# Kernel optimization log

Measured on AMD Instinct MI355X. Metric: run time of the kernel, lower is better.

## Reference

```python
import jax, jax.numpy as jnp
import numpy as np

B, T, D, TY = 64, 512, 96, 512
H, DK = 4, 32            # num_heads, embed_dim_per_head
E = H * DK               # embed_dim = 128
P = 2                    # function='L' -> 2 coefficients
L, HID = 64, 128         # latent_dim, hidden_dim


def setup_inputs() -> dict:
    key = jax.random.key(0)
    ks = jax.random.split(key, 16)
    inp = {
        "timesteps": jax.random.uniform(ks[0], (B, T), jnp.float32),
        "X": jax.random.normal(ks[1], (B, T, D), jnp.float32),
        "M": jax.random.randint(ks[2], (B, T, D), 0, 2).astype(jnp.float32),
        "y_time_steps": jax.random.uniform(ks[3], (B, TY), jnp.float32),
        # time_embedding: Linear(1, E)
        "te_w": jax.random.normal(ks[4], (E,), jnp.float32),
        "te_b": jax.random.normal(ks[5], (E,), jnp.float32) * 0.1,
        # learned query [1, P, E]
        "query": jax.random.normal(ks[6], (1, P, E), jnp.float32),
        # query_map / key_map: Linear(E, E), stored [in, out]
        "q_w": jax.random.normal(ks[7], (E, E), jnp.float32) / np.sqrt(E),
        "q_b": jax.random.normal(ks[8], (E,), jnp.float32) * 0.1,
        "k_w": jax.random.normal(ks[9], (E, E), jnp.float32) / np.sqrt(E),
        "k_b": jax.random.normal(ks[10], (E,), jnp.float32) * 0.1,
        # attn shared out: Linear(2D*H, L)
        "ow": jax.random.normal(ks[11], (2 * D * H, L), jnp.float32) / np.sqrt(2 * D * H),
        "ob": jnp.zeros((L,), jnp.float32),
        # decoder MLP: Linear(L,HID)+ReLU+Linear(HID,D)
        "w1": jax.random.normal(ks[12], (L, HID), jnp.float32) / np.sqrt(L),
        "b1": jnp.zeros((HID,), jnp.float32),
        "w2": jax.random.normal(ks[13], (HID, D), jnp.float32) / np.sqrt(HID),
        "b2": jnp.zeros((D,), jnp.float32),
    }
    return inp


def _fld_forward(timesteps, X, M, y_time_steps, te_w, te_b, query,
                 q_w, q_b, k_w, k_b, ow, ob, w1, b1, w2, b2):
    b, t, d = X.shape
    # time embedding: Linear(1,E), sin applied to indices i % H == 0
    emb = timesteps[..., None] * te_w + te_b               # [B,T,E]
    sin_idx = (jnp.arange(E) % H) == 0
    emb = jnp.where(sin_idx, jnp.sin(emb), emb)

    X_cat = jnp.concatenate([X, M], axis=-1)               # [B,T,2D]
    M_cat = jnp.concatenate([M, M], axis=-1)               # [B,T,2D]

    q = query @ q_w + q_b                                   # [1,P,E]
    k = emb @ k_w + k_b                                     # [B,T,E]
    q = q.reshape(1, P, H, DK).transpose(0, 2, 1, 3)        # [1,H,P,dk]
    k = k.reshape(b, t, H, DK).transpose(0, 2, 1, 3)        # [B,H,T,dk]

    scores = jnp.einsum('xhpd,bhtd->bhpt', q, k) / np.sqrt(DK)  # [B,H,P,T]
    # broadcast over value feature dim, mask per-feature, softmax over T
    logits = jnp.where(M_cat[:, None, None, :, :] == 0, -jnp.inf,
                       scores[..., None])                   # [B,H,P,T,2D]
    p = jax.nn.softmax(logits, axis=-2)
    xa = jnp.einsum('bhptf,btf->bhpf', p, X_cat)            # [B,H,P,2D]
    xa = xa.transpose(0, 2, 1, 3).reshape(b, P, H * 2 * d)  # [B,P,H*2D]
    coeffs = xa @ ow + ob                                   # [B,P,L]

    # function 'L': linear in y_time_steps
    x = coeffs[:, 0][:, None, :] + y_time_steps[:, :, None] * coeffs[:, 1][:, None, :]
    h1 = jax.nn.relu(x @ w1 + b1)
    return h1 @ w2 + b2                                     # [B,TY,D]


def reference(timesteps, X, M, y_time_steps, te_w, te_b, query,
              q_w, q_b, k_w, k_b, ow, ob, w1, b1, w2, b2):
    return _fld_forward(timesteps, X, M, y_time_steps, te_w, te_b, query,
                        q_w, q_b, k_w, k_b, ow, ob, w1, b1, w2, b2)
```

## Files before the change

kernel.cpp:

```cpp
#include <hip/hip_runtime.h>
#include <math.h>

#define B_   64
#define T_   512
#define D_   96
#define TY_  512
#define H_   4
#define DK_  32
#define E_   128
#define P_   2
#define L_   64
#define HID_ 128

#define WS_W2Q   0
#define WS_BQ    1024
#define WS_OB2   1056
#define WS_PN    2048
#define WS_PD    395264
#define WS_AB    788480

__global__ __launch_bounds__(256) void kprep(
    const float* __restrict__ query, const float* __restrict__ q_w,
    const float* __restrict__ q_b,   const float* __restrict__ k_w,
    const float* __restrict__ k_b,   const float* __restrict__ ow,
    const float* __restrict__ ob,    float* __restrict__ ws)
{
    const int tid = threadIdx.x;
    if (blockIdx.x == 0) {
        __shared__ float qm[P_ * E_];
        {
            int p = tid >> 7, ep = tid & 127;
            float acc = q_b[ep];
            #pragma unroll 4
            for (int e = 0; e < E_; ++e)
                acc += query[p * E_ + e] * q_w[e * E_ + ep];
            qm[p * E_ + ep] = acc;
        }
        __syncthreads();
        const float rs = 0.17677669529663687f;
        for (int idx = tid; idx < E_ * 8; idx += 256) {
            int e = idx >> 3, hp = idx & 7, h = hp >> 1, p = hp & 1;
            float acc = 0.f;
            #pragma unroll
            for (int dk = 0; dk < DK_; ++dk)
                acc += k_w[e * E_ + h * DK_ + dk] * qm[p * E_ + h * DK_ + dk];
            ws[WS_W2Q + idx] = acc * rs;
        }
        if (tid < 8) {
            int hp = tid, h = hp >> 1, p = hp & 1;
            float acc = 0.f;
            #pragma unroll
            for (int dk = 0; dk < DK_; ++dk)
                acc += k_b[h * DK_ + dk] * qm[p * E_ + h * DK_ + dk];
            ws[WS_BQ + hp] = acc * rs;
        }
    } else {
        __shared__ float obred[4][64];
        int l = tid & 63, sl = tid >> 6;
        float acc = 0.f;
        #pragma unroll 4
        for (int j = 0; j < D_; ++j)
            acc += ow[(size_t)(sl * 2 * D_ + D_ + j) * L_ + l];
        obred[sl][l] = acc;
        __syncthreads();
        if (sl == 0)
            ws[WS_OB2 + l] = ob[l] + obred[0][l] + obred[1][l] + obred[2][l] + obred[3][l];
    }
}

__global__ __launch_bounds__(256) void kspool(
    const float* __restrict__ tsteps, const float* __restrict__ te_w,
    const float* __restrict__ te_b,   const float* __restrict__ X,
    const float* __restrict__ M,      float* __restrict__ ws)
{
    const int c = blockIdx.x, b = blockIdx.y, tid = threadIdx.x;
    __shared__ float w2q_s[E_ * 8];
    __shared__ float tw_s[E_], tb_s[E_], bq_s[8];
    __shared__ float w_s[64 * 8];
    __shared__ float red[96 * 17];

    #pragma unroll
    for (int i = 0; i < 4; ++i) w2q_s[tid + i * 256] = ws[WS_W2Q + tid + i * 256];
    if (tid < E_) { tw_s[tid] = te_w[tid]; tb_s[tid] = te_b[tid]; }
    if (tid < 8)  bq_s[tid] = ws[WS_BQ + tid];
    __syncthreads();

    {
        const int t = tid & 63, hpg = tid >> 6, hp0 = hpg * 2;
        const float tv = tsteps[b * T_ + c * 64 + t];
        float a0 = 0.f, a1 = 0.f;
        #pragma unroll 4
        for (int e = 0; e < E_; ++e) {
            float v = tv * tw_s[e] + tb_s[e];
            if ((e & 3) == 0) v = __sinf(v);
            float2 w = *(const float2*)&w2q_s[e * 8 + hp0];
            a0 += v * w.x;
            a1 += v * w.y;
        }
        w_s[t * 8 + hp0]     = __expf(a0 + bq_s[hp0]);
        w_s[t * 8 + hp0 + 1] = __expf(a1 + bq_s[hp0 + 1]);
    }
    __syncthreads();

    const int fid = tid & 127, slice = tid >> 7;
    float num[8] = {0.f, 0.f, 0.f, 0.f, 0.f, 0.f, 0.f, 0.f};
    float den[8] = {0.f, 0.f, 0.f, 0.f, 0.f, 0.f, 0.f, 0.f};
    if (fid < 96) {
        #pragma unroll 4
        for (int i = 0; i < 32; ++i) {
            int tl = slice + 2 * i;
            size_t base = ((size_t)(b * T_ + c * 64 + tl)) * D_ + fid;
            float m = M[base], x = X[base];
            float mx = m * x;
            const float* wr = w_s + tl * 8;
            #pragma unroll
            for (int hp = 0; hp < 8; ++hp) {
                num[hp] += wr[hp] * mx;
                den[hp] += wr[hp] * m;
            }
        }
    }
    __syncthreads();
    if (slice == 1 && fid < 96) {
        #pragma unroll
        for (int hp = 0; hp < 8; ++hp) {
            red[fid * 17 + hp]     = num[hp];
            red[fid * 17 + 8 + hp] = den[hp];
        }
    }
    __syncthreads();
    if (slice == 0 && fid < 96) {
        float* pN = ws + WS_PN + ((size_t)((b * 8 + c) * 8)) * 96;
        float* pD = ws + WS_PD + ((size_t)((b * 8 + c) * 8)) * 96;
        #pragma unroll
        for (int hp = 0; hp < 8; ++hp) {
            pN[hp * 96 + fid] = num[hp] + red[fid * 17 + hp];
            pD[hp * 96 + fid] = den[hp] + red[fid * 17 + 8 + hp];
        }
    }
}

__global__ __launch_bounds__(256) void kcoef(
    const float* __restrict__ ow, const float* __restrict__ w1,
    const float* __restrict__ b1, float* __restrict__ ws)
{
    const int b = blockIdx.x, tid = threadIdx.x;
    __shared__ float xa_s[8 * 96];
    __shared__ float cf_part[2 * 128];
    __shared__ float cf_s[2 * 64];

    for (int flat = tid; flat < 8 * 96; flat += 256) {
        int hp = flat / 96, f = flat - hp * 96;
        float n = 0.f, d = 0.f;
        #pragma unroll
        for (int c = 0; c < 8; ++c) {
            n += ws[WS_PN + ((size_t)((b * 8 + c) * 8 + hp)) * 96 + f];
            d += ws[WS_PD + ((size_t)((b * 8 + c) * 8 + hp)) * 96 + f];
        }
        xa_s[flat] = n / d;
    }
    __syncthreads();
    {
        int hh = tid >> 7, rem = tid & 127, p = rem >> 6, l = rem & 63;
        float acc = (hh == 0) ? ws[WS_OB2 + l] : 0.f;
        #pragma unroll
        for (int hi = 0; hi < 2; ++hi) {
            int h = hh * 2 + hi;
            const float* xr = xa_s + (h * 2 + p) * 96;
            const float* owr = ow + (size_t)(h * 2 * D_) * L_ + l;
            #pragma unroll 4
            for (int f = 0; f < 96; ++f)
                acc += xr[f] * owr[(size_t)f * L_];
        }
        cf_part[hh * 128 + rem] = acc;
    }
    __syncthreads();
    if (tid < 128) cf_s[tid] = cf_part[tid] + cf_part[128 + tid];
    __syncthreads();
    if (tid < 128) {
        int j = tid;
        float a0 = b1[j], a1 = 0.f;
        #pragma unroll 4
        for (int l = 0; l < 64; ++l) {
            float wv = w1[l * HID_ + j];
            a0 += cf_s[l] * wv;
            a1 += cf_s[64 + l] * wv;
        }
        ws[WS_AB + b * 256 + j] = a0;
        ws[WS_AB + b * 256 + 128 + j] = a1;
    }
}

__global__ __launch_bounds__(256) void kdec(
    const float* __restrict__ yts, const float* __restrict__ w2,
    const float* __restrict__ b2,  const float* __restrict__ ws,
    float* __restrict__ out)
{
    __shared__ float h_s[HID_ * 64];
    __shared__ float y_s[64];
    __shared__ float a0_s[HID_], a1_s[HID_];
    const int tid = threadIdx.x;
    const int posb = blockIdx.x * 64;
    const int b = posb >> 9;

    if (tid < 64) y_s[tid] = yts[posb + tid];
    if (tid >= 64 && tid < 192) {
        int j = tid - 64;
        a0_s[j] = ws[WS_AB + b * 256 + j];
        a1_s[j] = ws[WS_AB + b * 256 + 128 + j];
    }
    __syncthreads();

    #pragma unroll 4
    for (int r = 0; r < 32; ++r) {
        int flat = r * 256 + tid;
        int j = flat >> 6, pos = flat & 63;
        h_s[flat] = fmaxf(0.f, a0_s[j] + y_s[pos] * a1_s[j]);
    }
    __syncthreads();

    const int pg = tid >> 4, dg = tid & 15;
    const int p0 = pg * 4, d0 = dg * 6;
    float acc[4][6];
    #pragma unroll
    for (int pp = 0; pp < 4; ++pp)
        #pragma unroll
        for (int dd = 0; dd < 6; ++dd) acc[pp][dd] = 0.f;

    #pragma unroll 2
    for (int j = 0; j < HID_; ++j) {
        float4 h4 = *(const float4*)&h_s[j * 64 + p0];
        const float* wr = w2 + j * D_ + d0;
        float wv[6];
        #pragma unroll
        for (int dd = 0; dd < 6; ++dd) wv[dd] = wr[dd];
        const float hv[4] = {h4.x, h4.y, h4.z, h4.w};
        #pragma unroll
        for (int pp = 0; pp < 4; ++pp)
            #pragma unroll
            for (int dd = 0; dd < 6; ++dd)
                acc[pp][dd] += hv[pp] * wv[dd];
    }

    float bv[6];
    #pragma unroll
    for (int dd = 0; dd < 6; ++dd) bv[dd] = b2[d0 + dd];
    #pragma unroll
    for (int pp = 0; pp < 4; ++pp) {
        size_t ob = ((size_t)(posb + p0 + pp)) * D_ + d0;
        #pragma unroll
        for (int dd = 0; dd < 6; ++dd) out[ob + dd] = acc[pp][dd] + bv[dd];
    }
}

extern "C" void kernel_launch(void* const* d_in, const int* in_sizes, int n_in,
                              void* d_out, int out_size, void* d_ws, size_t ws_size,
                              hipStream_t stream)
{
    const float* timesteps = (const float*)d_in[0];
    const float* X         = (const float*)d_in[1];
    const float* M         = (const float*)d_in[2];
    const float* yts       = (const float*)d_in[3];
    const float* te_w      = (const float*)d_in[4];
    const float* te_b      = (const float*)d_in[5];
    const float* query     = (const float*)d_in[6];
    const float* q_w       = (const float*)d_in[7];
    const float* q_b       = (const float*)d_in[8];
    const float* k_w       = (const float*)d_in[9];
    const float* k_b       = (const float*)d_in[10];
    const float* ow        = (const float*)d_in[11];
    const float* ob        = (const float*)d_in[12];
    const float* w1        = (const float*)d_in[13];
    const float* b1        = (const float*)d_in[14];
    const float* w2        = (const float*)d_in[15];
    const float* b2        = (const float*)d_in[16];
    float* out = (float*)d_out;
    float* ws  = (float*)d_ws;

    kprep<<<2, 256, 0, stream>>>(query, q_w, q_b, k_w, k_b, ow, ob, ws);
    kspool<<<dim3(8, B_), 256, 0, stream>>>(timesteps, te_w, te_b, X, M, ws);
    kcoef<<<B_, 256, 0, stream>>>(ow, w1, b1, ws);
    kdec<<<(B_ * TY_) / 64, 256, 0, stream>>>(yts, w2, b2, ws, out);
}
```

Baseline: 164.3 us.

## Fold weight-prep kernel into spool and coef kernels, widen coef blocks

Removes the separate kprep launch. Each kspool block now recomputes the query projection and the folded key/query weights itself, and kcoef recomputes the ob2 bias term. kcoef moves to 512 threads and splits its matvecs into more partial sums. This saves one launch and its serial dependency, but adds redundant per-block weight math (512 spool blocks each redo a 128x128 matvec) and extra global reads of ow.

```diff
diff --git a/kernel.cpp b/kernel.cpp
--- a/kernel.cpp
+++ b/kernel.cpp
@@ -12,77 +12,54 @@
 #define L_   64
 #define HID_ 128
 
-#define WS_W2Q   0
-#define WS_BQ    1024
-#define WS_OB2   1056
 #define WS_PN    2048
 #define WS_PD    395264
 #define WS_AB    788480
 
-__global__ __launch_bounds__(256) void kprep(
-    const float* __restrict__ query, const float* __restrict__ q_w,
-    const float* __restrict__ q_b,   const float* __restrict__ k_w,
-    const float* __restrict__ k_b,   const float* __restrict__ ow,
-    const float* __restrict__ ob,    float* __restrict__ ws)
-{
-    const int tid = threadIdx.x;
-    if (blockIdx.x == 0) {
-        __shared__ float qm[P_ * E_];
-        {
-            int p = tid >> 7, ep = tid & 127;
-            float acc = q_b[ep];
-            #pragma unroll 4
-            for (int e = 0; e < E_; ++e)
-                acc += query[p * E_ + e] * q_w[e * E_ + ep];
-            qm[p * E_ + ep] = acc;
-        }
-        __syncthreads();
-        const float rs = 0.17677669529663687f;
-        for (int idx = tid; idx < E_ * 8; idx += 256) {
-            int e = idx >> 3, hp = idx & 7, h = hp >> 1, p = hp & 1;
-            float acc = 0.f;
-            #pragma unroll
-            for (int dk = 0; dk < DK_; ++dk)
-                acc += k_w[e * E_ + h * DK_ + dk] * qm[p * E_ + h * DK_ + dk];
-            ws[WS_W2Q + idx] = acc * rs;
-        }
-        if (tid < 8) {
-            int hp = tid, h = hp >> 1, p = hp & 1;
-            float acc = 0.f;
-            #pragma unroll
-            for (int dk = 0; dk < DK_; ++dk)
-                acc += k_b[h * DK_ + dk] * qm[p * E_ + h * DK_ + dk];
-            ws[WS_BQ + hp] = acc * rs;
-        }
-    } else {
-        __shared__ float obred[4][64];
-        int l = tid & 63, sl = tid >> 6;
-        float acc = 0.f;
-        #pragma unroll 4
-        for (int j = 0; j < D_; ++j)
-            acc += ow[(size_t)(sl * 2 * D_ + D_ + j) * L_ + l];
-        obred[sl][l] = acc;
-        __syncthreads();
-        if (sl == 0)
-            ws[WS_OB2 + l] = ob[l] + obred[0][l] + obred[1][l] + obred[2][l] + obred[3][l];
-    }
-}
-
 __global__ __launch_bounds__(256) void kspool(
     const float* __restrict__ tsteps, const float* __restrict__ te_w,
     const float* __restrict__ te_b,   const float* __restrict__ X,
-    const float* __restrict__ M,      float* __restrict__ ws)
+    const float* __restrict__ M,      const float* __restrict__ query,
+    const float* __restrict__ q_w,    const float* __restrict__ q_b,
+    const float* __restrict__ k_w,    const float* __restrict__ k_b,
+    float* __restrict__ ws)
 {
     const int c = blockIdx.x, b = blockIdx.y, tid = threadIdx.x;
+    __shared__ float qm[P_ * E_];
     __shared__ float w2q_s[E_ * 8];
     __shared__ float tw_s[E_], tb_s[E_], bq_s[8];
     __shared__ float w_s[64 * 8];
     __shared__ float red[96 * 17];
 
-    #pragma unroll
-    for (int i = 0; i < 4; ++i) w2q_s[tid + i * 256] = ws[WS_W2Q + tid + i * 256];
+    {
+        int p = tid >> 7, ep = tid & 127;
+        float acc = q_b[ep];
+        #pragma unroll 4
+        for (int e = 0; e < E_; ++e)
+            acc += query[p * E_ + e] * q_w[e * E_ + ep];
+        qm[p * E_ + ep] = acc;
+    }
     if (tid < E_) { tw_s[tid] = te_w[tid]; tb_s[tid] = te_b[tid]; }
-    if (tid < 8)  bq_s[tid] = ws[WS_BQ + tid];
+    __syncthreads();
+    const float rs = 0.17677669529663687f;
+    #pragma unroll
+    for (int i = 0; i < 4; ++i) {
+        int idx = tid + i * 256;
+        int e = idx >> 3, hp = idx & 7, h = hp >> 1, p = hp & 1;
+        float acc = 0.f;
+        #pragma unroll
+        for (int dk = 0; dk < DK_; ++dk)
+            acc += k_w[e * E_ + h * DK_ + dk] * qm[p * E_ + h * DK_ + dk];
+        w2q_s[idx] = acc * rs;
+    }
+    if (tid < 8) {
+        int hp = tid, h = hp >> 1, p = hp & 1;
+        float acc = 0.f;
+        #pragma unroll
+        for (int dk = 0; dk < DK_; ++dk)
+            acc += k_b[h * DK_ + dk] * qm[p * E_ + h * DK_ + dk];
+        bq_s[hp] = acc * rs;
+    }
     __syncthreads();
 
     {
@@ -140,16 +117,19 @@
     }
 }
 
-__global__ __launch_bounds__(256) void kcoef(
+__global__ __launch_bounds__(512) void kcoef(
     const float* __restrict__ ow, const float* __restrict__ w1,
-    const float* __restrict__ b1, float* __restrict__ ws)
+    const float* __restrict__ b1, const float* __restrict__ ob,
+    float* __restrict__ ws)
 {
     const int b = blockIdx.x, tid = threadIdx.x;
     __shared__ float xa_s[8 * 96];
-    __shared__ float cf_part[2 * 128];
-    __shared__ float cf_s[2 * 64];
-
-    for (int flat = tid; flat < 8 * 96; flat += 256) {
+    __shared__ float obp[8][64];
+    __shared__ float cfp[4][2][64];
+    __shared__ float cf_s[2][64];
+    __shared__ float abp[4][2][128];
+
+    for (int flat = tid; flat < 8 * 96; flat += 512) {
         int hp = flat / 96, f = flat - hp * 96;
         float n = 0.f, d = 0.f;
         #pragma unroll
@@ -159,35 +139,59 @@
         }
         xa_s[flat] = n / d;
     }
-    __syncthreads();
-    {
-        int hh = tid >> 7, rem = tid & 127, p = rem >> 6, l = rem & 63;
-        float acc = (hh == 0) ? ws[WS_OB2 + l] : 0.f;
-        #pragma unroll
-        for (int hi = 0; hi < 2; ++hi) {
-            int h = hh * 2 + hi;
-            const float* xr = xa_s + (h * 2 + p) * 96;
-            const float* owr = ow + (size_t)(h * 2 * D_) * L_ + l;
-            #pragma unroll 4
-            for (int f = 0; f < 96; ++f)
-                acc += xr[f] * owr[(size_t)f * L_];
-        }
-        cf_part[hh * 128 + rem] = acc;
-    }
-    __syncthreads();
-    if (tid < 128) cf_s[tid] = cf_part[tid] + cf_part[128 + tid];
-    __syncthreads();
+    {
+        int g = tid >> 6, l = tid & 63;
+        float acc = 0.f;
+        #pragma unroll 4
+        for (int k = 0; k < 48; ++k) {
+            int hj = g * 48 + k, h = hj / 96, j = hj - h * 96;
+            acc += ow[(size_t)(h * 2 * D_ + D_ + j) * L_ + l];
+        }
+        obp[g][l] = acc;
+    }
+    __syncthreads();
+
+    {
+        int h = tid >> 7, p = (tid >> 6) & 1, l = tid & 63;
+        const float* xr = xa_s + (h * 2 + p) * 96;
+        const float* owr = ow + (size_t)(h * 2 * D_) * L_ + l;
+        float acc = 0.f;
+        #pragma unroll 4
+        for (int f = 0; f < 96; ++f)
+            acc += xr[f] * owr[(size_t)f * L_];
+        cfp[h][p][l] = acc;
+    }
+    __syncthreads();
+
     if (tid < 128) {
-        int j = tid;
-        float a0 = b1[j], a1 = 0.f;
-        #pragma unroll 4
-        for (int l = 0; l < 64; ++l) {
+        int p = tid >> 6, l = tid & 63;
+        float v = cfp[0][p][l] + cfp[1][p][l] + cfp[2][p][l] + cfp[3][p][l] + ob[l];
+        #pragma unroll
+        for (int g = 0; g < 8; ++g) v += obp[g][l];
+        cf_s[p][l] = v;
+    }
+    __syncthreads();
+
+    {
+        int s = tid >> 7, j = tid & 127;
+        float a0 = 0.f, a1 = 0.f;
+        #pragma unroll
+        for (int li = 0; li < 16; ++li) {
+            int l = s * 16 + li;
             float wv = w1[l * HID_ + j];
-            a0 += cf_s[l] * wv;
-            a1 += cf_s[64 + l] * wv;
-        }
-        ws[WS_AB + b * 256 + j] = a0;
-        ws[WS_AB + b * 256 + 128 + j] = a1;
+            a0 += cf_s[0][l] * wv;
+            a1 += cf_s[1][l] * wv;
+        }
+        abp[s][0][j] = a0;
+        abp[s][1][j] = a1;
+    }
+    __syncthreads();
+
+    if (tid < 256) {
+        int q = tid >> 7, j = tid & 127;
+        float v = abp[0][q][j] + abp[1][q][j] + abp[2][q][j] + abp[3][q][j];
+        if (q == 0) v += b1[j];
+        ws[WS_AB + b * 256 + q * 128 + j] = v;
     }
 }
 
@@ -277,8 +281,8 @@
     float* out = (float*)d_out;
     float* ws  = (float*)d_ws;
 
-    kprep<<<2, 256, 0, stream>>>(query, q_w, q_b, k_w, k_b, ow, ob, ws);
-    kspool<<<dim3(8, B_), 256, 0, stream>>>(timesteps, te_w, te_b, X, M, ws);
-    kcoef<<<B_, 256, 0, stream>>>(ow, w1, b1, ws);
+    kspool<<<dim3(8, B_), 256, 0, stream>>>(timesteps, te_w, te_b, X, M,
+                                            query, q_w, q_b, k_w, k_b, ws);
+    kcoef<<<B_, 512, 0, stream>>>(ow, w1, b1, ob, ws);
     kdec<<<(B_ * TY_) / 64, 256, 0, stream>>>(yts, w2, b2, ws, out);
 }
```

Result: no change. 165.4 us (+0.7%).
